# Kernel tuning notes

Hardware: AMD Instinct MI355X
Metric: run time of the kernel (lower is better)

The kernel has to match this reference:

```python
import jax, jax.numpy as jnp
import numpy as np

B, NS, NN = 1024, 1, 64
F = 128            # feat_dim = edge_dim = time_dim = pos_dim
DM = 4 * F         # model_dim = 512
H, DK = 2, 256     # n_head, d_k = d_v = model_dim // n_head
LN_EPS = 1e-5


def setup_inputs() -> dict:
    key = jax.random.key(0)
    ks = jax.random.split(key, 20)
    s = 0.02
    inp = {
        'src':   jax.random.normal(ks[0], (B, NS, F), jnp.float32),
        'src_t': jax.random.normal(ks[1], (B, NS, F), jnp.float32),
        'src_p': jax.random.normal(ks[2], (B, NS, F), jnp.float32),
        'seq':   jax.random.normal(ks[3], (B, NN, F), jnp.float32),
        'seq_t': jax.random.normal(ks[4], (B, NN, F), jnp.float32),
        'seq_e': jax.random.normal(ks[5], (B, NN, F), jnp.float32),
        'seq_p': jax.random.normal(ks[6], (B, NN, F), jnp.float32),
        'mask':  jax.random.randint(ks[7], (B, NS, NN), 0, 2).astype(bool),
        # MapBasedMultiHeadAttention params
        'wq': jax.random.normal(ks[8], (H * DK, DM), jnp.float32) * s,
        'wk': jax.random.normal(ks[9], (H * DK, DM), jnp.float32) * s,
        'wv': jax.random.normal(ks[10], (H * DK, DM), jnp.float32) * s,
        'wm': jax.random.normal(ks[11], (2 * DK,), jnp.float32) * s,   # weight_map: Linear(2*d_k, 1, bias=False)
        'fc_w': jax.random.normal(ks[12], (DM, H * DK), jnp.float32) * s,
        'fc_b': jnp.zeros((DM,), jnp.float32),
        'ln_g': jnp.ones((DM,), jnp.float32),
        'ln_b': jnp.zeros((DM,), jnp.float32),
        # MergeLayer(model_dim, feat_dim, feat_dim, feat_dim)
        'm1_w': jax.random.normal(ks[13], (F, DM + F), jnp.float32) * s,
        'm1_b': jnp.zeros((F,), jnp.float32),
        'm2_w': jax.random.normal(ks[14], (F, F), jnp.float32) * s,
        'm2_b': jnp.zeros((F,), jnp.float32),
    }
    return inp


def reference(src, src_t, src_p, seq, seq_t, seq_e, seq_p, mask,
              wq, wk, wv, wm, fc_w, fc_b, ln_g, ln_b, m1_w, m1_b, m2_w, m2_b):
    b, ns, f = src.shape
    nn = seq.shape[1]
    src_e = jnp.zeros((b, ns, f), src.dtype)  # edge feats of sources are zero
    q = jnp.concatenate([src, src_e, src_t, src_p], axis=-1)   # [B,NS,DM]
    k = jnp.concatenate([seq, seq_e, seq_t, seq_p], axis=-1)   # [B,NN,DM]

    # per-head projections: weight [H*DK, DM] -> [H, DK, DM]
    qh = jnp.einsum('bsd,hed->bshe', q, wq.reshape(H, DK, DM))  # [B,NS,H,DK]
    kh = jnp.einsum('bnd,hed->bnhe', k, wk.reshape(H, DK, DM))  # [B,NN,H,DK]
    vh = jnp.einsum('bnd,hed->bnhe', k, wv.reshape(H, DK, DM))  # [B,NN,H,DK]

    # weight_map(Linear over concat([q,k])) == q @ wm[:DK] + k @ wm[DK:]
    score_q = jnp.einsum('bshe,e->bhs', qh, wm[:DK])            # [B,H,NS]
    score_k = jnp.einsum('bnhe,e->bhn', kh, wm[DK:])            # [B,H,NN]
    attn = score_q[..., None] + score_k[:, :, None, :]          # [B,H,NS,NN]
    attn = jnp.where(mask[:, None, :, :], jnp.float32(-1e10), attn)
    attn = jax.nn.softmax(attn, axis=-1)

    out = jnp.einsum('bhsn,bnhe->bshe', attn, vh).reshape(b, ns, H * DK)
    out = jnp.einsum('bsd,ed->bse', out, fc_w) + fc_b           # fc
    out = jnp.where(out >= 0, out, 0.2 * out)                   # LeakyReLU(0.2)
    out = out + q                                               # residual
    mu = out.mean(axis=-1, keepdims=True)
    var = out.var(axis=-1, keepdims=True)
    out = (out - mu) / jnp.sqrt(var + LN_EPS) * ln_g + ln_b     # LayerNorm

    # MergeLayer (non_linear=True)
    x = jnp.concatenate([out, src], axis=-1)                    # [B,NS,DM+F]
    hdn = jax.nn.relu(jnp.einsum('bsd,ed->bse', x, m1_w) + m1_b)
    z = jnp.einsum('bsd,ed->bse', hdn, m2_w) + m2_b             # [B,NS,F]

    # attn in original layout: [n_head*B, len_q, len_k]
    attn_flat = attn.transpose(1, 0, 2, 3).reshape(H * b, ns, nn)
    return (z, attn_flat)
```

## Files before the change

kernel.cpp:

```cpp
#include <hip/hip_runtime.h>
#include <hip/hip_bf16.h>
#include <stdint.h>

#define B_   1024
#define NN_  64
#define F_   128
#define DM_  512
#define DK_  256

typedef unsigned short u16;
using f32x4  = __attribute__((ext_vector_type(4))) float;
using bf16x8 = __attribute__((ext_vector_type(8))) short;

__device__ __forceinline__ uint32_t f2bf(float x) {
  uint32_t u = __builtin_bit_cast(uint32_t, x);
  return (u + 0x7fffu + ((u >> 16) & 1u)) >> 16;
}
__device__ __forceinline__ float bf2f(uint32_t us) {
  return __builtin_bit_cast(float, us << 16);
}
__device__ __forceinline__ void split_pack(float x, float y, uint32_t& hp, uint32_t& lp) {
  uint32_t hx = f2bf(x), hy = f2bf(y);
  uint32_t lx = f2bf(x - bf2f(hx)), ly = f2bf(y - bf2f(hy));
  hp = hx | (hy << 16);
  lp = lx | (ly << 16);
}
__device__ __forceinline__ void split1(float x, u16& h, u16& l) {
  uint32_t hx = f2bf(x);
  h = (u16)hx;
  l = (u16)f2bf(x - bf2f(hx));
}
template <int CTRL>
__device__ __forceinline__ float dppadd(float x) {
  int r = __builtin_amdgcn_mov_dpp(__builtin_bit_cast(int, x), CTRL, 0xF, 0xF, true);
  return x + __builtin_bit_cast(float, r);
}

__global__ __launch_bounds__(256) void k_prep(
    const float* __restrict__ wv, const float* __restrict__ fc_w,
    const float* __restrict__ m1_w, const float* __restrict__ m2_w,
    const float* __restrict__ wk, const float* __restrict__ wm,
    u16* __restrict__ fc_hi, u16* __restrict__ fc_lo,
    u16* __restrict__ wvT_hi, u16* __restrict__ wvT_lo,
    u16* __restrict__ m1_hi, u16* __restrict__ m1_lo,
    u16* __restrict__ m2_hi, u16* __restrict__ m2_lo,
    float* __restrict__ wkc) {
  __shared__ float tile[32][33];
  int tid = threadIdx.x;
  int bx = blockIdx.x;

  if (bx >= 256) {
    int t = bx - 256;
    int h = t >> 3, dc = t & 7;
    int w = tid >> 6, l = tid & 63;
    int d = dc * 64 + l;
    const float* base = wk + (size_t)(h * DK_ + w * 64) * DM_ + d;
    float sacc[8] = {0.f, 0.f, 0.f, 0.f, 0.f, 0.f, 0.f, 0.f};
    #pragma unroll
    for (int e = 0; e < 64; ++e)
      sacc[e & 7] += base[e * DM_] * wm[DK_ + w * 64 + e];
    float s = ((sacc[0] + sacc[1]) + (sacc[2] + sacc[3])) +
              ((sacc[4] + sacc[5]) + (sacc[6] + sacc[7]));
    float* part = &tile[0][0];
    part[w * 64 + l] = s;
    __syncthreads();
    if (w == 0)
      wkc[h * DM_ + d] = part[l] + part[64 + l] + part[128 + l] + part[192 + l];
    return;
  }

  int gtid = bx * 256 + tid;
  int nthr = 256 * 256;
  for (int i = gtid; i < DM_ * DM_; i += nthr) split1(fc_w[i], fc_hi[i], fc_lo[i]);
  for (int i = gtid; i < F_ * (DM_ + F_); i += nthr) split1(m1_w[i], m1_hi[i], m1_lo[i]);
  for (int i = gtid; i < F_ * F_; i += nthr) split1(m2_w[i], m2_hi[i], m2_lo[i]);

  int e0 = (bx >> 4) * 32, d0 = (bx & 15) * 32;
  int rr = tid >> 3, c4 = (tid & 7) * 4;
  float4 v = *(const float4*)(wv + (e0 + rr) * DM_ + d0 + c4);
  tile[rr][c4] = v.x; tile[rr][c4 + 1] = v.y;
  tile[rr][c4 + 2] = v.z; tile[rr][c4 + 3] = v.w;
  __syncthreads();
  int dr = tid >> 3, ec = (tid & 7) * 4;
  #pragma unroll
  for (int q = 0; q < 4; ++q) {
    int idx = (d0 + dr) * DM_ + e0 + ec + q;
    split1(tile[ec + q][dr], wvT_hi[idx], wvT_lo[idx]);
  }
}

__device__ __forceinline__ f32x4 mfma_tile_split(
    const u16* __restrict__ Ahi, const u16* __restrict__ Alo, int lda,
    const u16* __restrict__ Bhi, const u16* __restrict__ Blo, int ldb, int K) {
  int l = threadIdx.x & 63;
  int r = l & 15, g = l >> 4;
  int offA = r * lda + g * 8;
  int offB = r * ldb + g * 8;
  f32x4 acc = {0.f, 0.f, 0.f, 0.f};
  for (int k = 0; k < K; k += 32) {
    bf16x8 ah = *(const bf16x8*)(Ahi + offA + k);
    bf16x8 al = *(const bf16x8*)(Alo + offA + k);
    bf16x8 bh = *(const bf16x8*)(Bhi + offB + k);
    bf16x8 bl = *(const bf16x8*)(Blo + offB + k);
    acc = __builtin_amdgcn_mfma_f32_16x16x32_bf16(ah, bh, acc, 0, 0, 0);
    acc = __builtin_amdgcn_mfma_f32_16x16x32_bf16(ah, bl, acc, 0, 0, 0);
    acc = __builtin_amdgcn_mfma_f32_16x16x32_bf16(al, bh, acc, 0, 0, 0);
  }
  return acc;
}

__global__ __launch_bounds__(256) void k_wcomb(
    const u16* __restrict__ fc_hi, const u16* __restrict__ fc_lo,
    const u16* __restrict__ wvT_hi, const u16* __restrict__ wvT_lo,
    u16* __restrict__ wc_hi, u16* __restrict__ wc_lo) {
  int wid = threadIdx.x >> 6;
  int n0g = blockIdx.y * 32;
  int h = n0g >> 9, d0 = n0g & 511;
  int m0 = blockIdx.x * 32 + (wid >> 1) * 16;
  int nb = d0 + (wid & 1) * 16;
  f32x4 acc = mfma_tile_split(fc_hi + m0 * DM_ + h * DK_,
                              fc_lo + m0 * DM_ + h * DK_, DM_,
                              wvT_hi + nb * DM_ + h * DK_,
                              wvT_lo + nb * DM_ + h * DK_, DM_, DK_);
  int l = threadIdx.x & 63, r = l & 15, g = l >> 4;
  #pragma unroll
  for (int i = 0; i < 4; ++i) {
    int m = m0 + g * 4 + i;
    int idx = m * 1024 + n0g + (wid & 1) * 16 + r;
    split1(acc[i], wc_hi[idx], wc_lo[idx]);
  }
}

__global__ __launch_bounds__(256, 2) void k_attn(
    const float* __restrict__ seq, const float* __restrict__ seq_e,
    const float* __restrict__ seq_t, const float* __restrict__ seq_p,
    const int* __restrict__ mask, const float* __restrict__ wkc,
    float* __restrict__ attn_out,
    uint32_t* __restrict__ kbar_hi, uint32_t* __restrict__ kbar_lo) {
  __shared__ float pbuf[4][2][64][17];
  __shared__ float attns[2][64];
  int tid = threadIdx.x, b = blockIdx.x;
  int w = tid >> 6, i = tid & 63;

  const float* arr = (w == 0 ? seq : (w == 1 ? seq_e : (w == 2 ? seq_t : seq_p)));
  const float* base = arr + (size_t)b * (64 * 128) + 2 * i;
  float c00 = wkc[w * 128 + 2 * i],       c01 = wkc[w * 128 + 2 * i + 1];
  float c10 = wkc[512 + w * 128 + 2 * i], c11 = wkc[512 + w * 128 + 2 * i + 1];

  float kx[64], ky[64];
  #pragma unroll
  for (int j = 0; j < 64; ++j) {
    float2 v = *(const float2*)(base + j * 128);
    kx[j] = v.x; ky[j] = v.y;
  }
  #pragma unroll
  for (int j = 0; j < 64; ++j) {
    float p0 = kx[j] * c00 + ky[j] * c01;
    float p1 = kx[j] * c10 + ky[j] * c11;
    p0 = dppadd<0xB1>(p0); p0 = dppadd<0x4E>(p0);
    p1 = dppadd<0xB1>(p1); p1 = dppadd<0x4E>(p1);
    if ((i & 3) == 0) {
      pbuf[w][0][j][i >> 2] = p0;
      pbuf[w][1][j][i >> 2] = p1;
    }
  }
  __syncthreads();

  if (tid < 128) {
    int h = w;
    float s = 0.f;
    #pragma unroll
    for (int w4 = 0; w4 < 4; ++w4)
      #pragma unroll
      for (int gq = 0; gq < 16; ++gq) s += pbuf[w4][h][i][gq];
    if (mask[b * 64 + i]) s = -1e10f;
    float m = s;
    #pragma unroll
    for (int off = 32; off; off >>= 1) m = fmaxf(m, __shfl_xor(m, off));
    float p = expf(s - m);
    float ssum = p;
    #pragma unroll
    for (int off = 32; off; off >>= 1) ssum += __shfl_xor(ssum, off);
    float a = p / ssum;
    attns[h][i] = a;
    attn_out[(h * B_ + b) * 64 + i] = a;
  }
  __syncthreads();

  float a00 = 0.f, a01 = 0.f, a10 = 0.f, a11 = 0.f;
  #pragma unroll
  for (int j = 0; j < 64; ++j) {
    float t0 = attns[0][j], t1 = attns[1][j];
    a00 += t0 * kx[j]; a01 += t0 * ky[j];
    a10 += t1 * kx[j]; a11 += t1 * ky[j];
  }
  uint32_t hp, lp;
  int idx = b * 512 + w * 64 + i;
  split_pack(a00, a01, hp, lp);
  kbar_hi[idx] = hp; kbar_lo[idx] = lp;
  split_pack(a10, a11, hp, lp);
  kbar_hi[idx + 256] = hp; kbar_lo[idx + 256] = lp;
}

__global__ __launch_bounds__(256) void k_fc(
    const u16* __restrict__ kb_hi, const u16* __restrict__ kb_lo,
    const u16* __restrict__ wc_hi, const u16* __restrict__ wc_lo,
    const float* __restrict__ fc_b,
    const float* __restrict__ src, const float* __restrict__ src_t,
    const float* __restrict__ src_p, float* __restrict__ fco) {
  int tid = threadIdx.x;
  int wid = tid >> 6, l = tid & 63;
  int r = l & 15, g = l >> 4;
  int m0 = blockIdx.x * 32 + (wid >> 1) * 16;
  int n0 = blockIdx.y * 64 + (wid & 1) * 32;
  int offA  = (m0 + r) * 1024 + g * 8;
  int offB0 = (n0 + r) * 1024 + g * 8;
  int offB1 = offB0 + 16 * 1024;
  f32x4 acc0 = {0.f, 0.f, 0.f, 0.f}, acc1 = {0.f, 0.f, 0.f, 0.f};
  #pragma unroll 4
  for (int k = 0; k < 1024; k += 32) {
    bf16x8 ah  = *(const bf16x8*)(kb_hi + offA + k);
    bf16x8 al  = *(const bf16x8*)(kb_lo + offA + k);
    bf16x8 b0h = *(const bf16x8*)(wc_hi + offB0 + k);
    bf16x8 b0l = *(const bf16x8*)(wc_lo + offB0 + k);
    bf16x8 b1h = *(const bf16x8*)(wc_hi + offB1 + k);
    bf16x8 b1l = *(const bf16x8*)(wc_lo + offB1 + k);
    acc0 = __builtin_amdgcn_mfma_f32_16x16x32_bf16(ah, b0h, acc0, 0, 0, 0);
    acc0 = __builtin_amdgcn_mfma_f32_16x16x32_bf16(ah, b0l, acc0, 0, 0, 0);
    acc0 = __builtin_amdgcn_mfma_f32_16x16x32_bf16(al, b0h, acc0, 0, 0, 0);
    acc1 = __builtin_amdgcn_mfma_f32_16x16x32_bf16(ah, b1h, acc1, 0, 0, 0);
    acc1 = __builtin_amdgcn_mfma_f32_16x16x32_bf16(ah, b1l, acc1, 0, 0, 0);
    acc1 = __builtin_amdgcn_mfma_f32_16x16x32_bf16(al, b1h, acc1, 0, 0, 0);
  }
  #pragma unroll
  for (int f = 0; f < 2; ++f) {
    int col = n0 + f * 16 + r;
    int part = col >> 7, fc2 = col & 127;
    float bias = fc_b[col];
    const float* qsrc = (part == 0 ? src : (part == 2 ? src_t : src_p));
    #pragma unroll
    for (int i = 0; i < 4; ++i) {
      int m = m0 + g * 4 + i;
      float c = (f == 0 ? acc0[i] : acc1[i]) + bias;
      c = (c >= 0.f) ? c : 0.2f * c;
      float qv = (part == 1) ? 0.f : qsrc[m * 128 + fc2];
      fco[m * 512 + col] = c + qv;
    }
  }
}

__global__ __launch_bounds__(64) void k_ln(
    const float* __restrict__ fco, const float* __restrict__ ln_g,
    const float* __restrict__ ln_b, const float* __restrict__ src,
    u16* __restrict__ x_hi, u16* __restrict__ x_lo) {
  int b = blockIdx.x, l = threadIdx.x;
  float v[8];
  float s = 0.f, s2 = 0.f;
  #pragma unroll
  for (int j = 0; j < 8; ++j) {
    v[j] = fco[b * 512 + j * 64 + l];
    s += v[j]; s2 += v[j] * v[j];
  }
  #pragma unroll
  for (int off = 32; off; off >>= 1) { s += __shfl_xor(s, off); s2 += __shfl_xor(s2, off); }
  float mu = s * (1.f / 512.f);
  float var = s2 * (1.f / 512.f) - mu * mu;
  float rstd = rsqrtf(var + 1e-5f);
  #pragma unroll
  for (int j = 0; j < 8; ++j) {
    int idx = j * 64 + l;
    float o = (v[j] - mu) * rstd * ln_g[idx] + ln_b[idx];
    int xi = b * 640 + idx;
    split1(o, x_hi[xi], x_lo[xi]);
  }
  #pragma unroll
  for (int j = 0; j < 2; ++j) {
    int xi = b * 640 + 512 + j * 64 + l;
    split1(src[b * 128 + j * 64 + l], x_hi[xi], x_lo[xi]);
  }
}

__global__ __launch_bounds__(512) void k_m12(
    const u16* __restrict__ x_hi, const u16* __restrict__ x_lo,
    const u16* __restrict__ m1_hi, const u16* __restrict__ m1_lo,
    const float* __restrict__ m1_b,
    const u16* __restrict__ m2_hi, const u16* __restrict__ m2_lo,
    const float* __restrict__ m2_b, float* __restrict__ z) {
  __shared__ u16 hh[16][136], hl[16][136];
  int tid = threadIdx.x;
  int wid = tid >> 6, l = tid & 63;
  int r = l & 15, g = l >> 4;
  int m0 = blockIdx.x * 16;
  int nb = wid * 16;
  {
    f32x4 acc = mfma_tile_split(x_hi + m0 * 640, x_lo + m0 * 640, 640,
                                m1_hi + nb * 640, m1_lo + nb * 640, 640, 640);
    int col = nb + r;
    float bias = m1_b[col];
    #pragma unroll
    for (int ii = 0; ii < 4; ++ii) {
      int row = g * 4 + ii;
      float o = fmaxf(acc[ii] + bias, 0.f);
      split1(o, hh[row][col], hl[row][col]);
    }
  }
  __syncthreads();
  {
    f32x4 acc = mfma_tile_split(&hh[0][0], &hl[0][0], 136,
                                m2_hi + nb * 128, m2_lo + nb * 128, 128, 128);
    int col = nb + r;
    float bias = m2_b[col];
    #pragma unroll
    for (int ii = 0; ii < 4; ++ii) {
      int row = g * 4 + ii;
      z[(m0 + row) * 128 + col] = acc[ii] + bias;
    }
  }
}

extern "C" void kernel_launch(void* const* d_in, const int* in_sizes, int n_in,
                              void* d_out, int out_size, void* d_ws, size_t ws_size,
                              hipStream_t stream) {
  (void)in_sizes; (void)n_in; (void)out_size; (void)ws_size;
  const float* src   = (const float*)d_in[0];
  const float* src_t = (const float*)d_in[1];
  const float* src_p = (const float*)d_in[2];
  const float* seq   = (const float*)d_in[3];
  const float* seq_t = (const float*)d_in[4];
  const float* seq_e = (const float*)d_in[5];
  const float* seq_p = (const float*)d_in[6];
  const int*   mask  = (const int*)d_in[7];
  const float* wk   = (const float*)d_in[9];
  const float* wv   = (const float*)d_in[10];
  const float* wm   = (const float*)d_in[11];
  const float* fc_w = (const float*)d_in[12];
  const float* fc_b = (const float*)d_in[13];
  const float* ln_g = (const float*)d_in[14];
  const float* ln_b = (const float*)d_in[15];
  const float* m1_w = (const float*)d_in[16];
  const float* m1_b = (const float*)d_in[17];
  const float* m2_w = (const float*)d_in[18];
  const float* m2_b = (const float*)d_in[19];

  float* z_out    = (float*)d_out;
  float* attn_out = z_out + B_ * F_;

  char* ws = (char*)d_ws;
  float* wkc     = (float*)(ws + 0);
  u16* fc_hi     = (u16*)(ws + 4096);
  u16* fc_lo     = (u16*)(ws + 528384);
  u16* m1_hi     = (u16*)(ws + 1052672);
  u16* m1_lo     = (u16*)(ws + 1216512);
  u16* m2_hi     = (u16*)(ws + 1380352);
  u16* m2_lo     = (u16*)(ws + 1413120);
  u16* wvT_hi    = (u16*)(ws + 1445888);
  u16* wvT_lo    = (u16*)(ws + 1970176);
  u16* wc_hi     = (u16*)(ws + 2494464);
  u16* wc_lo     = (u16*)(ws + 3543040);
  uint32_t* kbhi = (uint32_t*)(ws + 4591616);
  uint32_t* kblo = (uint32_t*)(ws + 6688768);
  float* fco     = (float*)(ws + 8785920);
  u16* x_hi      = (u16*)(ws + 10883072);
  u16* x_lo      = (u16*)(ws + 12193792);

  hipLaunchKernelGGL(k_prep, dim3(272), dim3(256), 0, stream,
                     wv, fc_w, m1_w, m2_w, wk, wm,
                     fc_hi, fc_lo, wvT_hi, wvT_lo,
                     m1_hi, m1_lo, m2_hi, m2_lo, wkc);
  hipLaunchKernelGGL(k_attn, dim3(1024), dim3(256), 0, stream,
                     seq, seq_e, seq_t, seq_p, mask, wkc,
                     attn_out, kbhi, kblo);
  hipLaunchKernelGGL(k_wcomb, dim3(16, 32), dim3(256), 0, stream,
                     fc_hi, fc_lo, wvT_hi, wvT_lo, wc_hi, wc_lo);
  hipLaunchKernelGGL(k_fc, dim3(32, 8), dim3(256), 0, stream,
                     (const u16*)kbhi, (const u16*)kblo, wc_hi, wc_lo, fc_b,
                     src, src_t, src_p, fco);
  hipLaunchKernelGGL(k_ln, dim3(1024), dim3(64), 0, stream,
                     fco, ln_g, ln_b, src, x_hi, x_lo);
  hipLaunchKernelGGL(k_m12, dim3(64), dim3(512), 0, stream,
                     x_hi, x_lo, m1_hi, m1_lo, m1_b, m2_hi, m2_lo, m2_b, z_out);
}
```

Measured before the change: 92.03 us.

## Stage K tile in swizzled LDS as bf16 instead of per-thread register arrays

The attention kernel now loads each batch's 64x512 key tile with float4 loads, packs it to bf16 and stores it in a swizzled LDS buffer. It then computes row scores by reading rows from LDS, replacing the per-thread 128-float register arrays and DPP cross-lane reductions. The attention-weighted sum reads the same LDS tile. This is meant to cut register pressure, simplify the reductions and coalesce the global loads. In exchange it uses a large LDS footprint, which may limit blocks per CU. It also rounds K to bf16 before both the score and weighted-sum steps, which risks accuracy.

```diff
diff --git a/kernel.cpp b/kernel.cpp
--- a/kernel.cpp
+++ b/kernel.cpp
@@ -19,6 +19,9 @@
 __device__ __forceinline__ float bf2f(uint32_t us) {
   return __builtin_bit_cast(float, us << 16);
 }
+__device__ __forceinline__ uint32_t packbf(float a, float b) {
+  return f2bf(a) | (f2bf(b) << 16);
+}
 __device__ __forceinline__ void split_pack(float x, float y, uint32_t& hp, uint32_t& lp) {
   uint32_t hx = f2bf(x), hy = f2bf(y);
   uint32_t lx = f2bf(x - bf2f(hx)), ly = f2bf(y - bf2f(hy));
@@ -29,11 +32,6 @@
   uint32_t hx = f2bf(x);
   h = (u16)hx;
   l = (u16)f2bf(x - bf2f(hx));
-}
-template <int CTRL>
-__device__ __forceinline__ float dppadd(float x) {
-  int r = __builtin_amdgcn_mov_dpp(__builtin_bit_cast(int, x), CTRL, 0xF, 0xF, true);
-  return x + __builtin_bit_cast(float, r);
 }
 
 __global__ __launch_bounds__(256) void k_prep(
@@ -131,49 +129,56 @@
   }
 }
 
-__global__ __launch_bounds__(256, 2) void k_attn(
+__global__ __launch_bounds__(256) void k_attn(
     const float* __restrict__ seq, const float* __restrict__ seq_e,
     const float* __restrict__ seq_t, const float* __restrict__ seq_p,
     const int* __restrict__ mask, const float* __restrict__ wkc,
     float* __restrict__ attn_out,
     uint32_t* __restrict__ kbar_hi, uint32_t* __restrict__ kbar_lo) {
-  __shared__ float pbuf[4][2][64][17];
+  __shared__ uint32_t kls[64][256];
+  __shared__ float wkcs[2][512];
+  __shared__ float pbufB[4][2][64];
   __shared__ float attns[2][64];
   int tid = threadIdx.x, b = blockIdx.x;
   int w = tid >> 6, i = tid & 63;
 
+  for (int q = tid; q < 1024; q += 256) ((float*)wkcs)[q] = wkc[q];
+
   const float* arr = (w == 0 ? seq : (w == 1 ? seq_e : (w == 2 ? seq_t : seq_p)));
-  const float* base = arr + (size_t)b * (64 * 128) + 2 * i;
-  float c00 = wkc[w * 128 + 2 * i],       c01 = wkc[w * 128 + 2 * i + 1];
-  float c10 = wkc[512 + w * 128 + 2 * i], c11 = wkc[512 + w * 128 + 2 * i + 1];
-
-  float kx[64], ky[64];
-  #pragma unroll
-  for (int j = 0; j < 64; ++j) {
-    float2 v = *(const float2*)(base + j * 128);
-    kx[j] = v.x; ky[j] = v.y;
-  }
-  #pragma unroll
-  for (int j = 0; j < 64; ++j) {
-    float p0 = kx[j] * c00 + ky[j] * c01;
-    float p1 = kx[j] * c10 + ky[j] * c11;
-    p0 = dppadd<0xB1>(p0); p0 = dppadd<0x4E>(p0);
-    p1 = dppadd<0xB1>(p1); p1 = dppadd<0x4E>(p1);
-    if ((i & 3) == 0) {
-      pbuf[w][0][j][i >> 2] = p0;
-      pbuf[w][1][j][i >> 2] = p1;
-    }
+  int half = i >> 5, lane32 = i & 31;
+  const float* base = arr + (size_t)b * 8192 + half * 128 + lane32 * 4;
+  int L0 = w * 64 + 2 * lane32;
+  #pragma unroll
+  for (int jj = 0; jj < 32; ++jj) {
+    int r = 2 * jj + half;
+    float4 v = *(const float4*)(base + jj * 256);
+    uint32_t u0 = packbf(v.x, v.y), u1 = packbf(v.z, v.w);
+    int phys = L0 ^ (r & 30);
+    uint32_t* p = &kls[r][phys];
+    p[0] = u0; p[1] = u1;
+  }
+  __syncthreads();
+
+  {
+    int row = i, sw = row & 30;
+    float s0 = 0.f, s1 = 0.f;
+    #pragma unroll
+    for (int cc = 0; cc < 64; ++cc) {
+      int c = w * 64 + cc;
+      uint32_t u = kls[row][c ^ sw];
+      float f0 = bf2f(u & 0xffffu), f1 = bf2f(u >> 16);
+      s0 += f0 * wkcs[0][2 * c] + f1 * wkcs[0][2 * c + 1];
+      s1 += f0 * wkcs[1][2 * c] + f1 * wkcs[1][2 * c + 1];
+    }
+    pbufB[w][0][row] = s0;
+    pbufB[w][1][row] = s1;
   }
   __syncthreads();
 
   if (tid < 128) {
-    int h = w;
-    float s = 0.f;
-    #pragma unroll
-    for (int w4 = 0; w4 < 4; ++w4)
-      #pragma unroll
-      for (int gq = 0; gq < 16; ++gq) s += pbuf[w4][h][i][gq];
-    if (mask[b * 64 + i]) s = -1e10f;
+    int h = w, row = i;
+    float s = pbufB[0][h][row] + pbufB[1][h][row] + pbufB[2][h][row] + pbufB[3][h][row];
+    if (mask[b * 64 + row]) s = -1e10f;
     float m = s;
     #pragma unroll
     for (int off = 32; off; off >>= 1) m = fmaxf(m, __shfl_xor(m, off));
@@ -182,24 +187,28 @@
     #pragma unroll
     for (int off = 32; off; off >>= 1) ssum += __shfl_xor(ssum, off);
     float a = p / ssum;
-    attns[h][i] = a;
-    attn_out[(h * B_ + b) * 64 + i] = a;
-  }
-  __syncthreads();
-
-  float a00 = 0.f, a01 = 0.f, a10 = 0.f, a11 = 0.f;
-  #pragma unroll
-  for (int j = 0; j < 64; ++j) {
-    float t0 = attns[0][j], t1 = attns[1][j];
-    a00 += t0 * kx[j]; a01 += t0 * ky[j];
-    a10 += t1 * kx[j]; a11 += t1 * ky[j];
-  }
-  uint32_t hp, lp;
-  int idx = b * 512 + w * 64 + i;
-  split_pack(a00, a01, hp, lp);
-  kbar_hi[idx] = hp; kbar_lo[idx] = lp;
-  split_pack(a10, a11, hp, lp);
-  kbar_hi[idx + 256] = hp; kbar_lo[idx + 256] = lp;
+    attns[h][row] = a;
+    attn_out[(h * B_ + b) * 64 + row] = a;
+  }
+  __syncthreads();
+
+  {
+    int L = tid;
+    float a00 = 0.f, a01 = 0.f, a10 = 0.f, a11 = 0.f;
+    #pragma unroll
+    for (int j = 0; j < 64; ++j) {
+      uint32_t u = kls[j][L ^ (j & 30)];
+      float f0 = bf2f(u & 0xffffu), f1 = bf2f(u >> 16);
+      float t0 = attns[0][j], t1 = attns[1][j];
+      a00 += t0 * f0; a01 += t0 * f1;
+      a10 += t1 * f0; a11 += t1 * f1;
+    }
+    uint32_t hp, lp;
+    split_pack(a00, a01, hp, lp);
+    kbar_hi[b * 512 + L] = hp; kbar_lo[b * 512 + L] = lp;
+    split_pack(a10, a11, hp, lp);
+    kbar_hi[b * 512 + 256 + L] = hp; kbar_lo[b * 512 + 256 + L] = lp;
+  }
 }
 
 __global__ __launch_bounds__(256) void k_fc(
```

Measured after the change: 100.0 us. 8.7% more time.

## Split attention scoring into a wide score kernel and fuse LayerNorm into merge layer

Applied to the files above, without the earlier changes.

The per-batch attention kernel, which held 128 K values per thread in registers, is split in two. A score kernel runs on a 1024x4 grid and uses float4 loads and DPP/shuffle reductions to write partial scores per feature part. A second kernel sums the partials, applies softmax, and re-reads seq to form the attention-weighted sums. The separate LayerNorm kernel is folded into the merge-layer kernel, which normalizes its 16 rows into shared memory before the MFMA. This aims for better parallelism and lower register pressure, and drops one launch plus the x_hi/x_lo round trip, at the cost of reading seq twice and an extra launch for the score kernel.

```diff
diff --git a/kernel.cpp b/kernel.cpp
--- a/kernel.cpp
+++ b/kernel.cpp
@@ -34,6 +34,13 @@
 __device__ __forceinline__ float dppadd(float x) {
   int r = __builtin_amdgcn_mov_dpp(__builtin_bit_cast(int, x), CTRL, 0xF, 0xF, true);
   return x + __builtin_bit_cast(float, r);
+}
+__device__ __forceinline__ float red16(float p) {
+  p = dppadd<0xB1>(p);
+  p = dppadd<0x4E>(p);
+  p = dppadd<0x114>(p);
+  p = dppadd<0x118>(p);
+  return p;
 }
 
 __global__ __launch_bounds__(256) void k_prep(
@@ -131,49 +138,55 @@
   }
 }
 
-__global__ __launch_bounds__(256, 2) void k_attn(
+__global__ __launch_bounds__(256) void k_score(
     const float* __restrict__ seq, const float* __restrict__ seq_e,
     const float* __restrict__ seq_t, const float* __restrict__ seq_p,
-    const int* __restrict__ mask, const float* __restrict__ wkc,
+    const float* __restrict__ wkc, float* __restrict__ S_part) {
+  int b = blockIdx.x, w = blockIdx.y;
+  int tid = threadIdx.x;
+  int ww = tid >> 6, l = tid & 63;
+  int half = l >> 5, l32 = l & 31;
+  const float* arr = (w == 0 ? seq : (w == 1 ? seq_e : (w == 2 ? seq_t : seq_p)));
+  int cb = 4 * l32;
+  float c00 = wkc[w * 128 + cb],     c01 = wkc[w * 128 + cb + 1];
+  float c02 = wkc[w * 128 + cb + 2], c03 = wkc[w * 128 + cb + 3];
+  float c10 = wkc[512 + w * 128 + cb],     c11 = wkc[512 + w * 128 + cb + 1];
+  float c12 = wkc[512 + w * 128 + cb + 2], c13 = wkc[512 + w * 128 + cb + 3];
+  const float* base = arr + (size_t)b * 8192 + (size_t)(ww * 16 + half) * 128 + cb;
+  size_t s0i = (((size_t)w * 1024 + b) * 2 + 0) * 64;
+  size_t s1i = (((size_t)w * 1024 + b) * 2 + 1) * 64;
+  #pragma unroll
+  for (int i = 0; i < 8; ++i) {
+    float4 v = *(const float4*)(base + i * 256);
+    float p0 = v.x * c00 + v.y * c01 + v.z * c02 + v.w * c03;
+    float p1 = v.x * c10 + v.y * c11 + v.z * c12 + v.w * c13;
+    p0 = red16(p0); p1 = red16(p1);
+    p0 += __shfl_xor(p0, 16);
+    p1 += __shfl_xor(p1, 16);
+    if (l32 == 12) {
+      int r = ww * 16 + 2 * i + half;
+      S_part[s0i + r] = p0;
+      S_part[s1i + r] = p1;
+    }
+  }
+}
+
+__global__ __launch_bounds__(256) void k_attn2(
+    const float* __restrict__ seq, const float* __restrict__ seq_e,
+    const float* __restrict__ seq_t, const float* __restrict__ seq_p,
+    const int* __restrict__ mask, const float* __restrict__ S_part,
     float* __restrict__ attn_out,
     uint32_t* __restrict__ kbar_hi, uint32_t* __restrict__ kbar_lo) {
-  __shared__ float pbuf[4][2][64][17];
   __shared__ float attns[2][64];
   int tid = threadIdx.x, b = blockIdx.x;
-  int w = tid >> 6, i = tid & 63;
-
-  const float* arr = (w == 0 ? seq : (w == 1 ? seq_e : (w == 2 ? seq_t : seq_p)));
-  const float* base = arr + (size_t)b * (64 * 128) + 2 * i;
-  float c00 = wkc[w * 128 + 2 * i],       c01 = wkc[w * 128 + 2 * i + 1];
-  float c10 = wkc[512 + w * 128 + 2 * i], c11 = wkc[512 + w * 128 + 2 * i + 1];
-
-  float kx[64], ky[64];
-  #pragma unroll
-  for (int j = 0; j < 64; ++j) {
-    float2 v = *(const float2*)(base + j * 128);
-    kx[j] = v.x; ky[j] = v.y;
-  }
-  #pragma unroll
-  for (int j = 0; j < 64; ++j) {
-    float p0 = kx[j] * c00 + ky[j] * c01;
-    float p1 = kx[j] * c10 + ky[j] * c11;
-    p0 = dppadd<0xB1>(p0); p0 = dppadd<0x4E>(p0);
-    p1 = dppadd<0xB1>(p1); p1 = dppadd<0x4E>(p1);
-    if ((i & 3) == 0) {
-      pbuf[w][0][j][i >> 2] = p0;
-      pbuf[w][1][j][i >> 2] = p1;
-    }
-  }
-  __syncthreads();
 
   if (tid < 128) {
-    int h = w;
+    int h = tid >> 6, row = tid & 63;
     float s = 0.f;
     #pragma unroll
     for (int w4 = 0; w4 < 4; ++w4)
-      #pragma unroll
-      for (int gq = 0; gq < 16; ++gq) s += pbuf[w4][h][i][gq];
-    if (mask[b * 64 + i]) s = -1e10f;
+      s += S_part[(((size_t)w4 * 1024 + b) * 2 + h) * 64 + row];
+    if (mask[b * 64 + row]) s = -1e10f;
     float m = s;
     #pragma unroll
     for (int off = 32; off; off >>= 1) m = fmaxf(m, __shfl_xor(m, off));
@@ -182,20 +195,25 @@
     #pragma unroll
     for (int off = 32; off; off >>= 1) ssum += __shfl_xor(ssum, off);
     float a = p / ssum;
-    attns[h][i] = a;
-    attn_out[(h * B_ + b) * 64 + i] = a;
+    attns[h][row] = a;
+    attn_out[(h * B_ + b) * 64 + row] = a;
   }
   __syncthreads();
 
+  int part = tid >> 6, dp = tid & 63;
+  const float* colp =
+      (part == 0 ? seq : (part == 1 ? seq_e : (part == 2 ? seq_t : seq_p))) +
+      (size_t)b * 8192 + 2 * dp;
   float a00 = 0.f, a01 = 0.f, a10 = 0.f, a11 = 0.f;
   #pragma unroll
   for (int j = 0; j < 64; ++j) {
+    float2 v = *(const float2*)(colp + j * 128);
     float t0 = attns[0][j], t1 = attns[1][j];
-    a00 += t0 * kx[j]; a01 += t0 * ky[j];
-    a10 += t1 * kx[j]; a11 += t1 * ky[j];
+    a00 += t0 * v.x; a01 += t0 * v.y;
+    a10 += t1 * v.x; a11 += t1 * v.y;
   }
   uint32_t hp, lp;
-  int idx = b * 512 + w * 64 + i;
+  int idx = b * 512 + tid;
   split_pack(a00, a01, hp, lp);
   kbar_hi[idx] = hp; kbar_lo[idx] = lp;
   split_pack(a10, a11, hp, lp);
@@ -249,51 +267,55 @@
   }
 }
 
-__global__ __launch_bounds__(64) void k_ln(
+__global__ __launch_bounds__(512) void k_m12(
     const float* __restrict__ fco, const float* __restrict__ ln_g,
     const float* __restrict__ ln_b, const float* __restrict__ src,
-    u16* __restrict__ x_hi, u16* __restrict__ x_lo) {
-  int b = blockIdx.x, l = threadIdx.x;
-  float v[8];
-  float s = 0.f, s2 = 0.f;
-  #pragma unroll
-  for (int j = 0; j < 8; ++j) {
-    v[j] = fco[b * 512 + j * 64 + l];
-    s += v[j]; s2 += v[j] * v[j];
-  }
-  #pragma unroll
-  for (int off = 32; off; off >>= 1) { s += __shfl_xor(s, off); s2 += __shfl_xor(s2, off); }
-  float mu = s * (1.f / 512.f);
-  float var = s2 * (1.f / 512.f) - mu * mu;
-  float rstd = rsqrtf(var + 1e-5f);
-  #pragma unroll
-  for (int j = 0; j < 8; ++j) {
-    int idx = j * 64 + l;
-    float o = (v[j] - mu) * rstd * ln_g[idx] + ln_b[idx];
-    int xi = b * 640 + idx;
-    split1(o, x_hi[xi], x_lo[xi]);
-  }
-  #pragma unroll
-  for (int j = 0; j < 2; ++j) {
-    int xi = b * 640 + 512 + j * 64 + l;
-    split1(src[b * 128 + j * 64 + l], x_hi[xi], x_lo[xi]);
-  }
-}
-
-__global__ __launch_bounds__(512) void k_m12(
-    const u16* __restrict__ x_hi, const u16* __restrict__ x_lo,
     const u16* __restrict__ m1_hi, const u16* __restrict__ m1_lo,
     const float* __restrict__ m1_b,
     const u16* __restrict__ m2_hi, const u16* __restrict__ m2_lo,
     const float* __restrict__ m2_b, float* __restrict__ z) {
+  __shared__ u16 xh[16][648], xl[16][648];
   __shared__ u16 hh[16][136], hl[16][136];
   int tid = threadIdx.x;
+  int m0 = blockIdx.x * 16;
+
+  {
+    int row = tid >> 5, l32 = tid & 31;
+    int grow = m0 + row;
+    float v[16];
+    float s = 0.f, s2 = 0.f;
+    #pragma unroll
+    for (int q = 0; q < 16; ++q) {
+      v[q] = fco[grow * 512 + q * 32 + l32];
+      s += v[q]; s2 += v[q] * v[q];
+    }
+    #pragma unroll
+    for (int off = 16; off; off >>= 1) {
+      s += __shfl_xor(s, off, 32);
+      s2 += __shfl_xor(s2, off, 32);
+    }
+    float mu = s * (1.f / 512.f);
+    float var = s2 * (1.f / 512.f) - mu * mu;
+    float rstd = rsqrtf(var + 1e-5f);
+    #pragma unroll
+    for (int q = 0; q < 16; ++q) {
+      int col = q * 32 + l32;
+      float o = (v[q] - mu) * rstd * ln_g[col] + ln_b[col];
+      split1(o, xh[row][col], xl[row][col]);
+    }
+    #pragma unroll
+    for (int q2 = 0; q2 < 4; ++q2) {
+      int c = q2 * 32 + l32;
+      split1(src[grow * 128 + c], xh[row][512 + c], xl[row][512 + c]);
+    }
+  }
+  __syncthreads();
+
   int wid = tid >> 6, l = tid & 63;
   int r = l & 15, g = l >> 4;
-  int m0 = blockIdx.x * 16;
   int nb = wid * 16;
   {
-    f32x4 acc = mfma_tile_split(x_hi + m0 * 640, x_lo + m0 * 640, 640,
+    f32x4 acc = mfma_tile_split(&xh[0][0], &xl[0][0], 648,
                                 m1_hi + nb * 640, m1_lo + nb * 640, 640, 640);
     int col = nb + r;
     float bias = m1_b[col];
@@ -305,6 +327,7 @@
     }
   }
   __syncthreads();
+
   {
     f32x4 acc = mfma_tile_split(&hh[0][0], &hl[0][0], 136,
                                 m2_hi + nb * 128, m2_lo + nb * 128, 128, 128);
@@ -360,23 +383,23 @@
   uint32_t* kbhi = (uint32_t*)(ws + 4591616);
   uint32_t* kblo = (uint32_t*)(ws + 6688768);
   float* fco     = (float*)(ws + 8785920);
-  u16* x_hi      = (u16*)(ws + 10883072);
-  u16* x_lo      = (u16*)(ws + 12193792);
+  float* S_part  = (float*)(ws + 10883072);
 
   hipLaunchKernelGGL(k_prep, dim3(272), dim3(256), 0, stream,
                      wv, fc_w, m1_w, m2_w, wk, wm,
                      fc_hi, fc_lo, wvT_hi, wvT_lo,
                      m1_hi, m1_lo, m2_hi, m2_lo, wkc);
-  hipLaunchKernelGGL(k_attn, dim3(1024), dim3(256), 0, stream,
-                     seq, seq_e, seq_t, seq_p, mask, wkc,
+  hipLaunchKernelGGL(k_score, dim3(1024, 4), dim3(256), 0, stream,
+                     seq, seq_e, seq_t, seq_p, wkc, S_part);
+  hipLaunchKernelGGL(k_attn2, dim3(1024), dim3(256), 0, stream,
+                     seq, seq_e, seq_t, seq_p, mask, S_part,
                      attn_out, kbhi, kblo);
   hipLaunchKernelGGL(k_wcomb, dim3(16, 32), dim3(256), 0, stream,
                      fc_hi, fc_lo, wvT_hi, wvT_lo, wc_hi, wc_lo);
   hipLaunchKernelGGL(k_fc, dim3(32, 8), dim3(256), 0, stream,
                      (const u16*)kbhi, (const u16*)kblo, wc_hi, wc_lo, fc_b,
                      src, src_t, src_p, fco);
-  hipLaunchKernelGGL(k_ln, dim3(1024), dim3(64), 0, stream,
-                     fco, ln_g, ln_b, src, x_hi, x_lo);
   hipLaunchKernelGGL(k_m12, dim3(64), dim3(512), 0, stream,
-                     x_hi, x_lo, m1_hi, m1_lo, m1_b, m2_hi, m2_lo, m2_b, z_out);
-}
+                     fco, ln_g, ln_b, src,
+                     m1_hi, m1_lo, m1_b, m2_hi, m2_lo, m2_b, z_out);
+}
```

New measurement: 97.70 us. 6.2% more time.
